# Performance work log

Hardware: AMD Instinct MI355X
Metric: run time of the kernel (lower is better)

The kernel has to match this reference:

```python
import jax, jax.numpy as jnp
import numpy as np

N1, N2, N3, N4 = 50_000, 100_000, 200_000, 400_000
D, OUT = 128, 128


def silu(x):
    return x * jax.nn.sigmoid(x)


def mlp(h, Wa, ba, Wb, bb):
    # torch.nn.Sequential(Linear, SiLU, Linear)
    return silu(h @ Wa + ba) @ Wb + bb


def setup_inputs() -> dict:
    key = jax.random.key(0)
    ks = jax.random.split(key, 12)
    s = 1.0 / np.sqrt(D).astype(np.float32)
    inp = {
        "feat": jax.random.normal(ks[0], (N1, D), jnp.float32),
        "W1a": jax.random.normal(ks[1], (D, D), jnp.float32) * s,
        "b1a": jnp.zeros((D,), jnp.float32),
        "W1b": jax.random.normal(ks[2], (D, D), jnp.float32) * s,
        "b1b": jnp.zeros((D,), jnp.float32),
        "W2a": jax.random.normal(ks[3], (D, D), jnp.float32) * s,
        "b2a": jnp.zeros((D,), jnp.float32),
        "W2b": jax.random.normal(ks[4], (D, D), jnp.float32) * s,
        "b2b": jnp.zeros((D,), jnp.float32),
        "W3a": jax.random.normal(ks[5], (D, D), jnp.float32) * s,
        "b3a": jnp.zeros((D,), jnp.float32),
        "W3b": jax.random.normal(ks[6], (D, D), jnp.float32) * s,
        "b3b": jnp.zeros((D,), jnp.float32),
        "Wo": jax.random.normal(ks[7], (3 * D, OUT), jnp.float32) * (1.0 / np.sqrt(3 * D).astype(np.float32)),
        "bo": jnp.zeros((OUT,), jnp.float32),
        # n{k-1}_in_n{k} edges: each level-k path has exactly 2 subpath children
        "src12": jax.random.randint(ks[8], (2 * N2,), 0, N1),
        "dst12": jnp.repeat(jnp.arange(N2), 2),
        "src23": jax.random.randint(ks[9], (2 * N3,), 0, N2),
        "dst23": jnp.repeat(jnp.arange(N3), 2),
        "src34": jax.random.randint(ks[10], (2 * N4,), 0, N3),
        "dst34": jnp.repeat(jnp.arange(N4), 2),
    }
    return inp


def reference(feat, W1a, b1a, W1b, b1b, W2a, b2a, W2b, b2b,
              W3a, b3a, W3b, b3b, Wo, bo,
              src12, dst12, src23, dst23, src34, dst34):
    # ---- upward ----
    h1 = mlp(feat, W1a, b1a, W1b, b1b)                       # n1 features (kept for final concat)
    h2 = jax.ops.segment_prod(h1[src12], dst12, num_segments=N2, indices_are_sorted=True)
    h2t = mlp(h2, W2a, b2a, W2b, b2b)
    h3 = jax.ops.segment_prod(h2t[src23], dst23, num_segments=N3, indices_are_sorted=True)
    h3t = mlp(h3, W3a, b3a, W3b, b3b)
    h4 = jax.ops.segment_prod(h3t[src34], dst34, num_segments=N4, indices_are_sorted=True)
    # ---- downward ----
    # n2_has_n1 (reverse of n1_in_n2): sum n2 features onto n1 -> 'h2'
    h2_on_n1 = jax.ops.segment_sum(h2t[dst12], src12, num_segments=N1)
    # n4_has_n3 then n3_has_n2 (overwrite h on lower level)
    h3_dn = jax.ops.segment_sum(h4[dst34], src34, num_segments=N3)
    h2_dn = jax.ops.segment_sum(h3_dn[dst23], src23, num_segments=N2)
    # n2_has_n1 again -> 'h_down'
    h_down = jax.ops.segment_sum(h2_dn[dst12], src12, num_segments=N1)
    # final per-node linear + SiLU on concat([h, h2, h_down])
    out = silu(jnp.concatenate([h1, h2_on_n1, h_down], axis=-1) @ Wo + bo)
    return out
```

## Files before the change

### kernel.cpp

```cpp
#include <hip/hip_runtime.h>

#define D 128
#define XSH 136

#define SHIFT 11
#define NPB   2048
#define EPT   8

typedef _Float16 f16;
typedef __attribute__((ext_vector_type(8))) _Float16 f16x8;
typedef __attribute__((ext_vector_type(4))) float    f32x4;

__device__ __forceinline__ float silu_f(float x) {
    return x / (1.0f + __expf(-x));
}

struct WPtrs { const float* s0; const float* s1; const float* s2;
               const float* s3; const float* s4; const float* s5; };
__global__ void wconv_all_kernel(WPtrs wp, const float* __restrict__ Wo, f16* __restrict__ WT)
{
    const int blk = blockIdx.x, t = threadIdx.x;
    if (blk < 384) {
        const int wid = blk >> 6;
        const int off = ((blk & 63) << 8) + t;
        const int n = off >> 7, k = off & 127;
        const float* s;
        switch (wid) {
            case 0: s = wp.s0; break;
            case 1: s = wp.s1; break;
            case 2: s = wp.s2; break;
            case 3: s = wp.s3; break;
            case 4: s = wp.s4; break;
            default: s = wp.s5; break;
        }
        WT[(wid << 14) + off] = (f16)s[(k << 7) + n];
    } else {
        const int off = ((blk - 384) << 8) + t;
        const int n = off / 384, k = off - n * 384;
        WT[(6 << 14) + off] = (f16)Wo[k * 128 + n];
    }
}

template<bool GATHER>
__launch_bounds__(256)
__global__ void mlp_mfma_kernel(const void* __restrict__ in_, const int* __restrict__ src,
                                const f16* __restrict__ WaT, const float* __restrict__ ba,
                                const f16* __restrict__ WbT, const float* __restrict__ bb,
                                f16* __restrict__ out, int nrows)
{
    __shared__ f16 xs[64][XSH];
    const int t = threadIdx.x;
    const int w = t >> 6, l = t & 63;
    const int cl = l & 15, kg = l >> 4;
    const int row0 = blockIdx.x * 64;

    f16x8 wa[2][4], wb[2][4];
    #pragma unroll
    for (int nt = 0; nt < 2; ++nt)
        #pragma unroll
        for (int kk = 0; kk < 4; ++kk) {
            const size_t o = (size_t)((w * 2 + nt) * 16 + cl) * D + kk * 32 + kg * 8;
            wa[nt][kk] = *(const f16x8*)(WaT + o);
            wb[nt][kk] = *(const f16x8*)(WbT + o);
        }

    {
        const int r = t >> 2, q = t & 3;
        const int g = row0 + r;
        f16* dst = &xs[r][q * 32];
        if (g < nrows) {
            if (GATHER) {
                const f16* in = (const f16*)in_;
                const int a = src[2 * g], b = src[2 * g + 1];
                const f16x8* pa = (const f16x8*)(in + (size_t)a * D + q * 32);
                const f16x8* pb = (const f16x8*)(in + (size_t)b * D + q * 32);
                #pragma unroll
                for (int i = 0; i < 4; ++i) {
                    f16x8 av = pa[i], bv = pb[i], hv;
                    #pragma unroll
                    for (int j = 0; j < 8; ++j) hv[j] = (f16)((float)av[j] * (float)bv[j]);
                    *(f16x8*)(dst + 8 * i) = hv;
                }
            } else {
                const float* in = (const float*)in_;
                const float4* p = (const float4*)(in + (size_t)g * D + q * 32);
                #pragma unroll
                for (int i = 0; i < 4; ++i) {
                    float4 v0 = p[2 * i], v1 = p[2 * i + 1];
                    f16x8 hv = {(f16)v0.x, (f16)v0.y, (f16)v0.z, (f16)v0.w,
                                (f16)v1.x, (f16)v1.y, (f16)v1.z, (f16)v1.w};
                    *(f16x8*)(dst + 8 * i) = hv;
                }
            }
        } else {
            f16x8 z = {};
            #pragma unroll
            for (int i = 0; i < 4; ++i) *(f16x8*)(dst + 8 * i) = z;
        }
    }
    __syncthreads();

    f32x4 acc[2][4];

    #pragma unroll
    for (int nt = 0; nt < 2; ++nt)
        #pragma unroll
        for (int m = 0; m < 4; ++m) acc[nt][m] = (f32x4){0.f, 0.f, 0.f, 0.f};
    #pragma unroll
    for (int m = 0; m < 4; ++m)
        #pragma unroll
        for (int kk = 0; kk < 4; ++kk) {
            const f16x8 a = *(const f16x8*)&xs[m * 16 + cl][kk * 32 + kg * 8];
            acc[0][m] = __builtin_amdgcn_mfma_f32_16x16x32_f16(a, wa[0][kk], acc[0][m], 0, 0, 0);
            acc[1][m] = __builtin_amdgcn_mfma_f32_16x16x32_f16(a, wa[1][kk], acc[1][m], 0, 0, 0);
        }
    __syncthreads();
    #pragma unroll
    for (int nt = 0; nt < 2; ++nt) {
        const float bv = ba[w * 32 + nt * 16 + cl];
        #pragma unroll
        for (int m = 0; m < 4; ++m)
            #pragma unroll
            for (int r2 = 0; r2 < 4; ++r2)
                xs[m * 16 + kg * 4 + r2][w * 32 + nt * 16 + cl] = (f16)silu_f(acc[nt][m][r2] + bv);
    }
    __syncthreads();

    #pragma unroll
    for (int nt = 0; nt < 2; ++nt)
        #pragma unroll
        for (int m = 0; m < 4; ++m) acc[nt][m] = (f32x4){0.f, 0.f, 0.f, 0.f};
    #pragma unroll
    for (int m = 0; m < 4; ++m)
        #pragma unroll
        for (int kk = 0; kk < 4; ++kk) {
            const f16x8 a = *(const f16x8*)&xs[m * 16 + cl][kk * 32 + kg * 8];
            acc[0][m] = __builtin_amdgcn_mfma_f32_16x16x32_f16(a, wb[0][kk], acc[0][m], 0, 0, 0);
            acc[1][m] = __builtin_amdgcn_mfma_f32_16x16x32_f16(a, wb[1][kk], acc[1][m], 0, 0, 0);
        }
    __syncthreads();
    #pragma unroll
    for (int nt = 0; nt < 2; ++nt) {
        const float bv = bb[w * 32 + nt * 16 + cl];
        #pragma unroll
        for (int m = 0; m < 4; ++m)
            #pragma unroll
            for (int r2 = 0; r2 < 4; ++r2)
                xs[m * 16 + kg * 4 + r2][w * 32 + nt * 16 + cl] = (f16)(acc[nt][m][r2] + bv);
    }
    __syncthreads();

    {
        const int r = t >> 2, q = t & 3;
        const int g = row0 + r;
        if (g < nrows) {
            f16* dst = out + (size_t)g * D + q * 32;
            #pragma unroll
            for (int i = 0; i < 4; ++i)
                *(f16x8*)(dst + 8 * i) = *(const f16x8*)&xs[r][q * 32 + 8 * i];
        }
    }
}

__launch_bounds__(256)
__global__ void out_mfma_kernel(const f16* __restrict__ h1, const f16* __restrict__ h2on1,
                                const f16* __restrict__ hdown,
                                const f16* __restrict__ WoT, const float* __restrict__ bo,
                                float* __restrict__ out, int nrows)
{
    __shared__ f16 xs[64][XSH];
    const int t = threadIdx.x;
    const int w = t >> 6, l = t & 63;
    const int cl = l & 15, kg = l >> 4;
    const int row0 = blockIdx.x * 64;

    f32x4 acc[2][4];
    #pragma unroll
    for (int nt = 0; nt < 2; ++nt)
        #pragma unroll
        for (int m = 0; m < 4; ++m) acc[nt][m] = (f32x4){0.f, 0.f, 0.f, 0.f};

    const f16* parts[3] = {h1, h2on1, hdown};
    #pragma unroll
    for (int p = 0; p < 3; ++p) {
        f16x8 wo[2][4];
        #pragma unroll
        for (int nt = 0; nt < 2; ++nt)
            #pragma unroll
            for (int kk = 0; kk < 4; ++kk)
                wo[nt][kk] = *(const f16x8*)(WoT + (size_t)((w * 2 + nt) * 16 + cl) * 384
                                             + p * D + kk * 32 + kg * 8);
        {
            const int r = t >> 2, q = t & 3;
            const int g = row0 + r;
            f16* dst = &xs[r][q * 32];
            if (g < nrows) {
                const f16x8* pp = (const f16x8*)(parts[p] + (size_t)g * D + q * 32);
                #pragma unroll
                for (int i = 0; i < 4; ++i) *(f16x8*)(dst + 8 * i) = pp[i];
            } else {
                f16x8 z = {};
                #pragma unroll
                for (int i = 0; i < 4; ++i) *(f16x8*)(dst + 8 * i) = z;
            }
        }
        __syncthreads();
        #pragma unroll
        for (int m = 0; m < 4; ++m)
            #pragma unroll
            for (int kk = 0; kk < 4; ++kk) {
                const f16x8 a = *(const f16x8*)&xs[m * 16 + cl][kk * 32 + kg * 8];
                acc[0][m] = __builtin_amdgcn_mfma_f32_16x16x32_f16(a, wo[0][kk], acc[0][m], 0, 0, 0);
                acc[1][m] = __builtin_amdgcn_mfma_f32_16x16x32_f16(a, wo[1][kk], acc[1][m], 0, 0, 0);
            }
        __syncthreads();
    }

    #pragma unroll
    for (int nt = 0; nt < 2; ++nt) {
        const float bv = bo[w * 32 + nt * 16 + cl];
        #pragma unroll
        for (int m = 0; m < 4; ++m)
            #pragma unroll
            for (int r2 = 0; r2 < 4; ++r2) {
                const int g = row0 + m * 16 + kg * 4 + r2;
                if (g < nrows) out[(size_t)g * D + w * 32 + nt * 16 + cl] = silu_f(acc[nt][m][r2] + bv);
            }
    }
}


__global__ void bucket_hist_kernel(const int* __restrict__ s12, int E12,
                                   const int* __restrict__ s23, int E23,
                                   const int* __restrict__ s34, int E34,
                                   int* __restrict__ bcnt, int N1, int N2, int nbkt)
{
    __shared__ int h[256];
    const int t = threadIdx.x;
    for (int i = t; i < 256; i += blockDim.x) h[i] = 0;
    __syncthreads();
    const int Etot = E12 + E23 + E34;
    for (int g = blockIdx.x * blockDim.x + t; g < Etot; g += gridDim.x * blockDim.x) {
        int node;
        if (g < E12) node = s12[g];
        else if (g < E12 + E23) node = N1 + s23[g - E12];
        else node = N1 + N2 + s34[g - E12 - E23];
        atomicAdd(&h[node >> SHIFT], 1);
    }
    __syncthreads();
    for (int i = t; i < nbkt; i += blockDim.x)
        if (h[i]) atomicAdd(&bcnt[i], h[i]);
}

__global__ void bucket_scan_kernel(const int* __restrict__ bcnt, int* __restrict__ bbase,
                                   int* __restrict__ bcur, int nbkt, int Etot)
{
    __shared__ int s[256];
    const int t = threadIdx.x;
    const int v = (t < nbkt) ? bcnt[t] : 0;
    s[t] = v;
    __syncthreads();
    for (int d = 1; d < 256; d <<= 1) {
        const int u = (t >= d) ? s[t - d] : 0;
        __syncthreads();
        s[t] += u;
        __syncthreads();
    }
    if (t < nbkt) { const int ex = s[t] - v; bbase[t] = ex; bcur[t] = ex; }
    if (t == 0) bbase[nbkt] = Etot;
}

__global__ void csr_pass1_kernel(const int* __restrict__ s12, int E12,
                                 const int* __restrict__ s23, int E23,
                                 const int* __restrict__ s34, int E34,
                                 int* __restrict__ bcur, int2* __restrict__ recs,
                                 int N1, int N2, int nbkt)
{
    __shared__ int cnt[256];
    __shared__ int gbase[256];
    const int t = threadIdx.x;
    const int chunk = blockIdx.x * (256 * EPT);
    const int Etot = E12 + E23 + E34;
    for (int i = t; i < 256; i += 256) cnt[i] = 0;
    __syncthreads();
    int node_[EPT], pay_[EPT], br_[EPT];
    #pragma unroll
    for (int i = 0; i < EPT; ++i) {
        const int g = chunk + i * 256 + t;
        int node = -1, pay = 0, b = 0, r = 0;
        if (g < Etot) {
            if (g < E12) { node = s12[g]; pay = g >> 1; }
            else if (g < E12 + E23) { const int e = g - E12; node = N1 + s23[e]; pay = e >> 1; }
            else { const int e = g - E12 - E23; node = N1 + N2 + s34[e]; pay = s34[e ^ 1]; }
            b = node >> SHIFT;
            r = atomicAdd(&cnt[b], 1);
        }
        node_[i] = node; pay_[i] = pay; br_[i] = (b << 16) | r;
    }
    __syncthreads();
    if (t < nbkt && cnt[t]) gbase[t] = atomicAdd(&bcur[t], cnt[t]);
    __syncthreads();
    #pragma unroll
    for (int i = 0; i < EPT; ++i) {
        if (node_[i] >= 0) {
            const int b = br_[i] >> 16, r = br_[i] & 0xffff;
            recs[gbase[b] + r] = make_int2(node_[i], pay_[i]);
        }
    }
}

__launch_bounds__(1024)
__global__ void csr_pass2_kernel(const int2* __restrict__ recs,
                                 const int* __restrict__ bbase,
                                 int2* __restrict__ offcnt, int* __restrict__ el, int NT)
{
    __shared__ int cnt2[NPB];
    __shared__ int pref[NPB];
    __shared__ int s1[NPB / 2];
    const int b = blockIdx.x, t = threadIdx.x;
    const int node0 = b << SHIFT;
    const int k0 = bbase[b], k1 = bbase[b + 1];
    for (int i = t; i < NPB; i += 1024) cnt2[i] = 0;
    __syncthreads();
    for (int k = k0 + t; k < k1; k += 1024)
        atomicAdd(&cnt2[recs[k].x - node0], 1);
    __syncthreads();
    s1[t] = cnt2[2 * t] + cnt2[2 * t + 1];
    __syncthreads();
    for (int d = 1; d < 1024; d <<= 1) {
        const int u = (t >= d) ? s1[t - d] : 0;
        __syncthreads();
        s1[t] += u;
        __syncthreads();
    }
    {
        const int a = cnt2[2 * t];
        const int pairsum = a + cnt2[2 * t + 1];
        const int ex0 = s1[t] - pairsum;
        pref[2 * t] = ex0;
        pref[2 * t + 1] = ex0 + a;
    }
    __syncthreads();
    for (int i = t; i < NPB; i += 1024) {
        const int node = node0 + i;
        if (node < NT) offcnt[node] = make_int2(k0 + pref[i], cnt2[i]);
    }
    __syncthreads();
    for (int k = k0 + t; k < k1; k += 1024) {
        const int2 r = recs[k];
        const int pos = atomicAdd(&pref[r.x - node0], 1);
        el[k0 + pos] = r.y;
    }
}

__global__ void prod_gather_kernel(const f16* __restrict__ h3t,
                                   const int2* __restrict__ offcnt,
                                   const int* __restrict__ el,
                                   f16* __restrict__ h3dn, int nrows)
{
    const long long g = (long long)blockIdx.x * blockDim.x + threadIdx.x;
    const int i = (int)(g >> 4);
    if (i >= nrows) return;
    const int c = ((int)g & 15) * 8;
    const f16x8 ownv = *(const f16x8*)(h3t + (size_t)i * D + c);
    float acc0[8] = {}, acc1[8] = {};
    const int2 oc = offcnt[i];
    const int base = oc.x, deg = oc.y;
    int d = 0;
    for (; d + 2 <= deg; d += 2) {
        const int s0 = el[base + d], s1v = el[base + d + 1];
        const f16x8 v0 = *(const f16x8*)(h3t + (size_t)s0 * D + c);
        const f16x8 v1 = *(const f16x8*)(h3t + (size_t)s1v * D + c);
        #pragma unroll
        for (int j = 0; j < 8; ++j) { acc0[j] += (float)v0[j]; acc1[j] += (float)v1[j]; }
    }
    if (d < deg) {
        const int s0 = el[base + d];
        const f16x8 v0 = *(const f16x8*)(h3t + (size_t)s0 * D + c);
        #pragma unroll
        for (int j = 0; j < 8; ++j) acc0[j] += (float)v0[j];
    }
    f16x8 r;
    #pragma unroll
    for (int j = 0; j < 8; ++j) r[j] = (f16)((acc0[j] + acc1[j]) * (float)ownv[j]);
    *(f16x8*)(h3dn + (size_t)i * D + c) = r;
}

__global__ void gather_sum_kernel(const f16* __restrict__ val,
                                  const int2* __restrict__ offcnt,
                                  const int* __restrict__ el,
                                  f16* __restrict__ dst, int nrows)
{
    const long long g = (long long)blockIdx.x * blockDim.x + threadIdx.x;
    const int i = (int)(g >> 4);
    if (i >= nrows) return;
    const int c = ((int)g & 15) * 8;
    float acc0[8] = {}, acc1[8] = {};
    const int2 oc = offcnt[i];
    const int base = oc.x, deg = oc.y;
    int d = 0;
    for (; d + 2 <= deg; d += 2) {
        const int s0 = el[base + d], s1v = el[base + d + 1];
        const f16x8 v0 = *(const f16x8*)(val + (size_t)s0 * D + c);
        const f16x8 v1 = *(const f16x8*)(val + (size_t)s1v * D + c);
        #pragma unroll
        for (int j = 0; j < 8; ++j) { acc0[j] += (float)v0[j]; acc1[j] += (float)v1[j]; }
    }
    if (d < deg) {
        const int s0 = el[base + d];
        const f16x8 v0 = *(const f16x8*)(val + (size_t)s0 * D + c);
        #pragma unroll
        for (int j = 0; j < 8; ++j) acc0[j] += (float)v0[j];
    }
    f16x8 r;
    #pragma unroll
    for (int j = 0; j < 8; ++j) r[j] = (f16)(acc0[j] + acc1[j]);
    *(f16x8*)(dst + (size_t)i * D + c) = r;
}

__global__ void ws_report_kernel(float* out, float v) {
    if (threadIdx.x == 0 && blockIdx.x == 0) out[0] = v;
}

extern "C" void kernel_launch(void* const* d_in, const int* in_sizes, int n_in,
                              void* d_out, int out_size, void* d_ws, size_t ws_size,
                              hipStream_t stream)
{
    const float* feat = (const float*)d_in[0];
    const float* W1a = (const float*)d_in[1];  const float* b1a = (const float*)d_in[2];
    const float* W1b = (const float*)d_in[3];  const float* b1b = (const float*)d_in[4];
    const float* W2a = (const float*)d_in[5];  const float* b2a = (const float*)d_in[6];
    const float* W2b = (const float*)d_in[7];  const float* b2b = (const float*)d_in[8];
    const float* W3a = (const float*)d_in[9];  const float* b3a = (const float*)d_in[10];
    const float* W3b = (const float*)d_in[11]; const float* b3b = (const float*)d_in[12];
    const float* Wo  = (const float*)d_in[13]; const float* bo  = (const float*)d_in[14];
    const int* src12 = (const int*)d_in[15];
    const int* src23 = (const int*)d_in[17];
    const int* src34 = (const int*)d_in[19];

    const int N1 = in_sizes[0] / D;
    const int N2 = in_sizes[15] / 2;
    const int N3 = in_sizes[17] / 2;
    const int N4 = in_sizes[19] / 2;
    const int E12 = 2 * N2, E23 = 2 * N3, E34 = 2 * N4;
    const int NT = N1 + N2 + N3;
    const int Etot = E12 + E23 + E34;
    const int NBKT = (NT + NPB - 1) >> SHIFT;

    char* p = (char*)d_ws;
    f16* h1    = (f16*)p;  p += (size_t)N1 * D * sizeof(f16);
    f16* h2on1 = (f16*)p;  p += (size_t)N1 * D * sizeof(f16);
    f16* h2t   = (f16*)p;  p += (size_t)N2 * D * sizeof(f16);
    f16* h3t   = (f16*)p;  f16* h2dn  = h3t;
    p += (size_t)N3 * D * sizeof(f16);
    f16* h3dn  = (f16*)p;  f16* hdown = h3dn;
    p += (size_t)N3 * D * sizeof(f16);

    p = (char*)(((uintptr_t)p + 15) & ~(uintptr_t)15);
    int2* offcnt = (int2*)p;             p += (size_t)NT * sizeof(int2);
    int2* recs   = (int2*)p;             p += (size_t)Etot * sizeof(int2);
    int*  el     = (int*)p;              p += (size_t)Etot * sizeof(int);
    int*  bcnt   = (int*)p;              p += 256 * sizeof(int);
    int*  bbase  = (int*)p;              p += 257 * sizeof(int);
    int*  bcur   = (int*)p;              p += 256 * sizeof(int);

    p = (char*)(((uintptr_t)p + 31) & ~(uintptr_t)31);
    f16* WT = (f16*)p;
    f16* WaT1 = WT;
    f16* WbT1 = WaT1 + D * D;
    f16* WaT2 = WbT1 + D * D;
    f16* WbT2 = WaT2 + D * D;
    f16* WaT3 = WbT2 + D * D;
    f16* WbT3 = WaT3 + D * D;
    f16* WoT  = WbT3 + D * D;
    p = (char*)(WoT + 384 * D);

    const size_t need = p - (char*)d_ws;
    if (ws_size < need || NBKT > 256) {
        ws_report_kernel<<<1, 64, 0, stream>>>((float*)d_out, (float)ws_size);
        return;
    }

    dim3 blk(256);
    auto tiles    = [](int n) { return dim3((unsigned)((n + 63) / 64)); };
    auto rowblk16 = [](long long rows) { return dim3((unsigned)((rows * 16 + 255) / 256)); };

    WPtrs wp = {W1a, W1b, W2a, W2b, W3a, W3b};
    wconv_all_kernel<<<dim3(576), blk, 0, stream>>>(wp, Wo, WT);

    hipMemsetAsync(bcnt, 0, 256 * sizeof(int), stream);
    {
        const int nblk = (Etot + 2047) / 2048;
        bucket_hist_kernel<<<dim3((unsigned)nblk), blk, 0, stream>>>(
            src12, E12, src23, E23, src34, E34, bcnt, N1, N2, NBKT);
        bucket_scan_kernel<<<1, 256, 0, stream>>>(bcnt, bbase, bcur, NBKT, Etot);
        csr_pass1_kernel<<<dim3((unsigned)((Etot + 256 * EPT - 1) / (256 * EPT))), blk, 0, stream>>>(
            src12, E12, src23, E23, src34, E34, bcur, recs, N1, N2, NBKT);
        csr_pass2_kernel<<<dim3((unsigned)NBKT), dim3(1024), 0, stream>>>(
            recs, bbase, offcnt, el, NT);
    }

    mlp_mfma_kernel<false><<<tiles(N1), blk, 0, stream>>>(feat, nullptr, WaT1, b1a, WbT1, b1b, h1, N1);
    mlp_mfma_kernel<true ><<<tiles(N2), blk, 0, stream>>>(h1, src12, WaT2, b2a, WbT2, b2b, h2t, N2);
    gather_sum_kernel<<<rowblk16(N1), blk, 0, stream>>>(h2t, offcnt, el, h2on1, N1);
    mlp_mfma_kernel<true ><<<tiles(N3), blk, 0, stream>>>(h2t, src23, WaT3, b3a, WbT3, b3b, h3t, N3);

    prod_gather_kernel<<<rowblk16(N3), blk, 0, stream>>>(h3t, offcnt + N1 + N2, el, h3dn, N3);
    gather_sum_kernel<<<rowblk16(N2), blk, 0, stream>>>(h3dn, offcnt + N1, el, h2dn, N2);
    gather_sum_kernel<<<rowblk16(N1), blk, 0, stream>>>(h2dn, offcnt, el, hdown, N1);

    out_mfma_kernel<<<tiles(N1), blk, 0, stream>>>(h1, h2on1, hdown, WoT, bo, (float*)d_out, N1);
}
```

Before: 288.5 us.

## Swap MFMA operands for vectorized epilogue stores, double-buffer LDS, unroll gathers by four

```diff
diff --git a/kernel.cpp b/kernel.cpp
--- a/kernel.cpp
+++ b/kernel.cpp
@@ -8,6 +8,7 @@
 #define EPT   8
 
 typedef _Float16 f16;
+typedef __attribute__((ext_vector_type(4))) _Float16 f16x4;
 typedef __attribute__((ext_vector_type(8))) _Float16 f16x8;
 typedef __attribute__((ext_vector_type(4))) float    f32x4;
 
@@ -49,6 +50,7 @@
                                 f16* __restrict__ out, int nrows)
 {
     __shared__ f16 xs[64][XSH];
+    __shared__ f16 ys[64][XSH];
     const int t = threadIdx.x;
     const int w = t >> 6, l = t & 63;
     const int cl = l & 15, kg = l >> 4;
@@ -111,18 +113,22 @@
         #pragma unroll
         for (int kk = 0; kk < 4; ++kk) {
             const f16x8 a = *(const f16x8*)&xs[m * 16 + cl][kk * 32 + kg * 8];
-            acc[0][m] = __builtin_amdgcn_mfma_f32_16x16x32_f16(a, wa[0][kk], acc[0][m], 0, 0, 0);
-            acc[1][m] = __builtin_amdgcn_mfma_f32_16x16x32_f16(a, wa[1][kk], acc[1][m], 0, 0, 0);
-        }
-    __syncthreads();
+            acc[0][m] = __builtin_amdgcn_mfma_f32_16x16x32_f16(wa[0][kk], a, acc[0][m], 0, 0, 0);
+            acc[1][m] = __builtin_amdgcn_mfma_f32_16x16x32_f16(wa[1][kk], a, acc[1][m], 0, 0, 0);
+        }
     #pragma unroll
     for (int nt = 0; nt < 2; ++nt) {
-        const float bv = ba[w * 32 + nt * 16 + cl];
-        #pragma unroll
-        for (int m = 0; m < 4; ++m)
-            #pragma unroll
-            for (int r2 = 0; r2 < 4; ++r2)
-                xs[m * 16 + kg * 4 + r2][w * 32 + nt * 16 + cl] = (f16)silu_f(acc[nt][m][r2] + bv);
+        const int n0 = w * 32 + nt * 16 + kg * 4;
+        const float4 bv = *(const float4*)&ba[n0];
+        #pragma unroll
+        for (int m = 0; m < 4; ++m) {
+            f16x4 y;
+            y[0] = (f16)silu_f(acc[nt][m][0] + bv.x);
+            y[1] = (f16)silu_f(acc[nt][m][1] + bv.y);
+            y[2] = (f16)silu_f(acc[nt][m][2] + bv.z);
+            y[3] = (f16)silu_f(acc[nt][m][3] + bv.w);
+            *(f16x4*)&ys[m * 16 + cl][n0] = y;
+        }
     }
     __syncthreads();
 
@@ -134,19 +140,23 @@
     for (int m = 0; m < 4; ++m)
         #pragma unroll
         for (int kk = 0; kk < 4; ++kk) {
-            const f16x8 a = *(const f16x8*)&xs[m * 16 + cl][kk * 32 + kg * 8];
-            acc[0][m] = __builtin_amdgcn_mfma_f32_16x16x32_f16(a, wb[0][kk], acc[0][m], 0, 0, 0);
-            acc[1][m] = __builtin_amdgcn_mfma_f32_16x16x32_f16(a, wb[1][kk], acc[1][m], 0, 0, 0);
-        }
-    __syncthreads();
+            const f16x8 a = *(const f16x8*)&ys[m * 16 + cl][kk * 32 + kg * 8];
+            acc[0][m] = __builtin_amdgcn_mfma_f32_16x16x32_f16(wb[0][kk], a, acc[0][m], 0, 0, 0);
+            acc[1][m] = __builtin_amdgcn_mfma_f32_16x16x32_f16(wb[1][kk], a, acc[1][m], 0, 0, 0);
+        }
     #pragma unroll
     for (int nt = 0; nt < 2; ++nt) {
-        const float bv = bb[w * 32 + nt * 16 + cl];
-        #pragma unroll
-        for (int m = 0; m < 4; ++m)
-            #pragma unroll
-            for (int r2 = 0; r2 < 4; ++r2)
-                xs[m * 16 + kg * 4 + r2][w * 32 + nt * 16 + cl] = (f16)(acc[nt][m][r2] + bv);
+        const int n0 = w * 32 + nt * 16 + kg * 4;
+        const float4 bv = *(const float4*)&bb[n0];
+        #pragma unroll
+        for (int m = 0; m < 4; ++m) {
+            f16x4 z;
+            z[0] = (f16)(acc[nt][m][0] + bv.x);
+            z[1] = (f16)(acc[nt][m][1] + bv.y);
+            z[2] = (f16)(acc[nt][m][2] + bv.z);
+            z[3] = (f16)(acc[nt][m][3] + bv.w);
+            *(f16x4*)&xs[m * 16 + cl][n0] = z;
+        }
     }
     __syncthreads();
 
@@ -210,25 +220,29 @@
             #pragma unroll
             for (int kk = 0; kk < 4; ++kk) {
                 const f16x8 a = *(const f16x8*)&xs[m * 16 + cl][kk * 32 + kg * 8];
-                acc[0][m] = __builtin_amdgcn_mfma_f32_16x16x32_f16(a, wo[0][kk], acc[0][m], 0, 0, 0);
-                acc[1][m] = __builtin_amdgcn_mfma_f32_16x16x32_f16(a, wo[1][kk], acc[1][m], 0, 0, 0);
+                acc[0][m] = __builtin_amdgcn_mfma_f32_16x16x32_f16(wo[0][kk], a, acc[0][m], 0, 0, 0);
+                acc[1][m] = __builtin_amdgcn_mfma_f32_16x16x32_f16(wo[1][kk], a, acc[1][m], 0, 0, 0);
             }
         __syncthreads();
     }
 
     #pragma unroll
     for (int nt = 0; nt < 2; ++nt) {
-        const float bv = bo[w * 32 + nt * 16 + cl];
-        #pragma unroll
-        for (int m = 0; m < 4; ++m)
-            #pragma unroll
-            for (int r2 = 0; r2 < 4; ++r2) {
-                const int g = row0 + m * 16 + kg * 4 + r2;
-                if (g < nrows) out[(size_t)g * D + w * 32 + nt * 16 + cl] = silu_f(acc[nt][m][r2] + bv);
+        const int n0 = w * 32 + nt * 16 + kg * 4;
+        const float4 bv = *(const float4*)&bo[n0];
+        #pragma unroll
+        for (int m = 0; m < 4; ++m) {
+            const int g = row0 + m * 16 + cl;
+            if (g < nrows) {
+                float4 v = make_float4(silu_f(acc[nt][m][0] + bv.x),
+                                       silu_f(acc[nt][m][1] + bv.y),
+                                       silu_f(acc[nt][m][2] + bv.z),
+                                       silu_f(acc[nt][m][3] + bv.w));
+                *(float4*)(out + (size_t)g * D + n0) = v;
             }
-    }
-}
-
+        }
+    }
+}
 
 __global__ void bucket_hist_kernel(const int* __restrict__ s12, int E12,
                                    const int* __restrict__ s23, int E23,
@@ -367,14 +381,20 @@
     const int2 oc = offcnt[i];
     const int base = oc.x, deg = oc.y;
     int d = 0;
-    for (; d + 2 <= deg; d += 2) {
-        const int s0 = el[base + d], s1v = el[base + d + 1];
+    for (; d + 4 <= deg; d += 4) {
+        const int s0 = el[base + d + 0], s1v = el[base + d + 1];
+        const int s2 = el[base + d + 2], s3v = el[base + d + 3];
         const f16x8 v0 = *(const f16x8*)(h3t + (size_t)s0 * D + c);
         const f16x8 v1 = *(const f16x8*)(h3t + (size_t)s1v * D + c);
-        #pragma unroll
-        for (int j = 0; j < 8; ++j) { acc0[j] += (float)v0[j]; acc1[j] += (float)v1[j]; }
-    }
-    if (d < deg) {
+        const f16x8 v2 = *(const f16x8*)(h3t + (size_t)s2 * D + c);
+        const f16x8 v3 = *(const f16x8*)(h3t + (size_t)s3v * D + c);
+        #pragma unroll
+        for (int j = 0; j < 8; ++j) {
+            acc0[j] += (float)v0[j] + (float)v2[j];
+            acc1[j] += (float)v1[j] + (float)v3[j];
+        }
+    }
+    for (; d < deg; ++d) {
         const int s0 = el[base + d];
         const f16x8 v0 = *(const f16x8*)(h3t + (size_t)s0 * D + c);
         #pragma unroll
@@ -399,14 +419,20 @@
     const int2 oc = offcnt[i];
     const int base = oc.x, deg = oc.y;
     int d = 0;
-    for (; d + 2 <= deg; d += 2) {
-        const int s0 = el[base + d], s1v = el[base + d + 1];
+    for (; d + 4 <= deg; d += 4) {
+        const int s0 = el[base + d + 0], s1v = el[base + d + 1];
+        const int s2 = el[base + d + 2], s3v = el[base + d + 3];
         const f16x8 v0 = *(const f16x8*)(val + (size_t)s0 * D + c);
         const f16x8 v1 = *(const f16x8*)(val + (size_t)s1v * D + c);
-        #pragma unroll
-        for (int j = 0; j < 8; ++j) { acc0[j] += (float)v0[j]; acc1[j] += (float)v1[j]; }
-    }
-    if (d < deg) {
+        const f16x8 v2 = *(const f16x8*)(val + (size_t)s2 * D + c);
+        const f16x8 v3 = *(const f16x8*)(val + (size_t)s3v * D + c);
+        #pragma unroll
+        for (int j = 0; j < 8; ++j) {
+            acc0[j] += (float)v0[j] + (float)v2[j];
+            acc1[j] += (float)v1[j] + (float)v3[j];
+        }
+    }
+    for (; d < deg; ++d) {
         const int s0 = el[base + d];
         const f16x8 v0 = *(const f16x8*)(val + (size_t)s0 * D + c);
         #pragma unroll
```

Result: faster. 277.5 us (-3.8%).
